# Performance work log

Measured on AMD Instinct MI355X. Metric: run time of the kernel, lower is better.

The kernel has to match this reference:

```python
import jax, jax.numpy as jnp
import numpy as np

B, L, S, T_IP = 2, 4096, 77, 16
C, C_CROSS, H = 1280, 768, 20
DH = C // H
REGION_WEIGHT = 0.3  # scalar inside weight_func: bias = region_state * sigma * REGION_WEIGHT
IP_SCALE = 1.0


def setup_inputs() -> dict:
    key = jax.random.key(0)
    ks = jax.random.split(key, 11)
    def w(k, shape, s=0.02):
        return jax.random.normal(k, shape, dtype=jnp.float32) * s
    return {
        "hidden_states": jax.random.normal(ks[0], (B, L, C), dtype=jnp.float32),
        "encoder_hidden_states": jax.random.normal(ks[1], (B, S, C_CROSS), dtype=jnp.float32),
        "ip_hidden_states": jax.random.normal(ks[2], (B, T_IP, C_CROSS), dtype=jnp.float32),
        "region_state": jax.random.uniform(ks[3], (B, L, S), dtype=jnp.float32),
        "sigma": jnp.full((1,), 14.6, dtype=jnp.float32),
        "Wq": w(ks[4], (C, C)),
        "Wk": w(ks[5], (C_CROSS, C)),
        "Wv": w(ks[6], (C_CROSS, C)),
        "Wk_ip": w(ks[7], (C_CROSS, C)),
        "Wv_ip": w(ks[8], (C_CROSS, C)),
        "Wout": w(ks[9], (C, C)),
        "b_out": jnp.zeros((C,), dtype=jnp.float32),
    }


def _split_heads(x):
    # [B, T, C] -> [B, H, T, DH]
    b, t, _ = x.shape
    return x.reshape(b, t, H, DH).transpose(0, 2, 1, 3)


def reference(hidden_states, encoder_hidden_states, ip_hidden_states, region_state,
              sigma, Wq, Wk, Wv, Wk_ip, Wv_ip, Wout, b_out):
    residual = hidden_states
    scale = 1.0 / np.sqrt(DH).astype(np.float32)

    q = _split_heads(hidden_states @ Wq)            # [B,H,L,DH]
    k = _split_heads(encoder_hidden_states @ Wk)    # [B,H,S,DH]
    v = _split_heads(encoder_hidden_states @ Wv)    # [B,H,S,DH]

    # region-state-biased cross attention (manual softmax path)
    scores = jnp.einsum('bhld,bhsd->bhls', q, k) * scale  # [B,H,L,S]
    # weight_func(region_state, sigma, attn_weight) -> region_state * sigma * REGION_WEIGHT,
    # broadcast over heads (repeat_interleave B -> B*H in the original).
    bias = (region_state * sigma[0] * REGION_WEIGHT)[:, None, :, :]  # [B,1,L,S]
    attn = jax.nn.softmax(scores + bias, axis=-1)
    out = jnp.einsum('bhls,bhsd->bhld', attn, v)
    out = out.transpose(0, 2, 1, 3).reshape(B, L, C)

    # IP-adapter stream: standard SDPA against image-prompt tokens
    k_ip = _split_heads(ip_hidden_states @ Wk_ip)   # [B,H,T,DH]
    v_ip = _split_heads(ip_hidden_states @ Wv_ip)
    s_ip = jax.nn.softmax(jnp.einsum('bhld,bhtd->bhlt', q, k_ip) * scale, axis=-1)
    out_ip = jnp.einsum('bhlt,bhtd->bhld', s_ip, v_ip).transpose(0, 2, 1, 3).reshape(B, L, C)

    out = out + IP_SCALE * out_ip
    out = out @ Wout + b_out     # attn.to_out[0]; to_out[1] is dropout (identity at p=0)
    return out + residual
```

## Files before the change

### kernel.cpp

```cpp
#include <hip/hip_runtime.h>
#include <cstdint>
#include <cstddef>

#define B_   2
#define L_   4096
#define S_   77
#define TIP_ 16
#define C_   1280
#define CC_  768
#define H_   20

typedef unsigned short u16;
typedef unsigned int   u32;
typedef __attribute__((ext_vector_type(8))) short bf16x8;
typedef __attribute__((ext_vector_type(8))) unsigned short u16x8;
typedef __attribute__((ext_vector_type(4))) float f32x4;

__device__ __forceinline__ u16 f2bf(float x) {
  u32 u = __float_as_uint(x);
  u32 r = (u + 0x7fffu + ((u >> 16) & 1u)) >> 16;
  return (u16)r;
}

__device__ __forceinline__ void gload16(const u16* g, const u16* l) {
  __builtin_amdgcn_global_load_lds(
      (const __attribute__((address_space(1))) u32*)g,
      (__attribute__((address_space(3))) u32*)(uintptr_t)l, 16, 0, 0);
}

__device__ __forceinline__ void wg_barrier() {
  asm volatile("s_barrier" ::: "memory");
}
template<int N>
__device__ __forceinline__ void vm_wait() {
  asm volatile("s_waitcnt vmcnt(%0)" :: "i"(N) : "memory");
}

__global__ __launch_bounds__(256) void prep_all(
    const float* __restrict__ X, const float* __restrict__ enc, const float* __restrict__ ip,
    u16* __restrict__ Xbf, u16* __restrict__ encbf, u16* __restrict__ ipbf,
    const float* __restrict__ Wq,  const float* __restrict__ Wk,   const float* __restrict__ Wv,
    const float* __restrict__ Wkip,const float* __restrict__ Wvip, const float* __restrict__ Wout,
    u16* __restrict__ WqT, u16* __restrict__ WkT, u16* __restrict__ WvT,
    u16* __restrict__ WkipT, u16* __restrict__ WvipT, u16* __restrict__ WoutT) {
  __shared__ float tile[32][33];
  const int bid = blockIdx.x;
  if (bid < 2048) {
    const int nX = B_*L_*C_;
    const int nE = B_*S_*CC_;
    const int nI = B_*TIP_*CC_;
    const int total4 = (nX + nE + nI) >> 2;
    for (int i = bid*256 + threadIdx.x; i < total4; i += 2048*256) {
      int idx = i << 2;
      const float* src; u16* dst; int off;
      if (idx < nX)            { src = X;   dst = Xbf;   off = idx; }
      else if (idx < nX + nE)  { src = enc; dst = encbf; off = idx - nX; }
      else                     { src = ip;  dst = ipbf;  off = idx - nX - nE; }
      float4 v = *(const float4*)(src + off);
      ushort4 o;
      o.x = f2bf(v.x); o.y = f2bf(v.y); o.z = f2bf(v.z); o.w = f2bf(v.w);
      *(ushort4*)(dst + off) = o;
    }
    return;
  }
  int t = bid - 2048;
  const float* src; u16* dst; int K;
  if      (t < 1600) { src = Wq;   dst = WqT;   K = C_;  }
  else if (t < 2560) { src = Wk;   dst = WkT;   K = CC_; t -= 1600; }
  else if (t < 3520) { src = Wv;   dst = WvT;   K = CC_; t -= 2560; }
  else if (t < 4480) { src = Wkip; dst = WkipT; K = CC_; t -= 3520; }
  else if (t < 5440) { src = Wvip; dst = WvipT; K = CC_; t -= 4480; }
  else               { src = Wout; dst = WoutT; K = C_;  t -= 5440; }
  const int tileK = t / 40, tileN = t % 40;
  const int tx = threadIdx.x & 31, ty = threadIdx.x >> 5;
  const int k0 = tileK*32, n0 = tileN*32;
  #pragma unroll
  for (int r = 0; r < 32; r += 8)
    tile[ty + r][tx] = src[(size_t)(k0 + ty + r)*C_ + n0 + tx];
  __syncthreads();
  #pragma unroll
  for (int r = 0; r < 32; r += 8) {
    const int n = n0 + ty + r, k = k0 + tx;
    dst[(size_t)n*K + k] = f2bf(tile[tx][ty + r]);
  }
}

template<int BM, int MODE, typename OutT>
__device__ __forceinline__ void gemm_core(
    const u16* __restrict__ A, int lda, int M,
    const u16* __restrict__ BT, int K,
    OutT* __restrict__ Cm,
    const float* __restrict__ bias, const float* __restrict__ resid,
    int mt, int nt) {
  constexpr int MR  = BM / 64;
  constexpr int AIT = BM / 64;
  constexpr int LP  = AIT + 3;
  __shared__ u16 As[2][BM*64];
  __shared__ u16 Bs[2][160*64];
  const int tid  = threadIdx.x;
  const int lane = tid & 63, wave = tid >> 6;
  const int wr = wave >> 1, wc = wave & 1;
  const int lhi = lane >> 4, llo = lane & 15;
  const int lsw = llo & 7;

  f32x4 acc[MR][5] = {};

  auto stage = [&](int kt) {
    u16* Asb = As[kt & 1];
    u16* Bsb = Bs[kt & 1];
    #pragma unroll
    for (int it = 0; it < AIT; ++it) {
      const int chunk = it*512 + wave*64 + lane;
      const int r = chunk >> 3, c8 = chunk & 7;
      const int g8 = c8 ^ (r & 7);
      int row_g = mt*BM + r; row_g = (row_g < M) ? row_g : (M - 1);
      gload16(A + (size_t)row_g*lda + kt*64 + g8*8,
              Asb + (size_t)(it*512 + wave*64)*8);
    }
    #pragma unroll
    for (int it = 0; it < 2; ++it) {
      const int chunk = it*512 + wave*64 + lane;
      const int r = chunk >> 3, c8 = chunk & 7;
      const int g8 = c8 ^ (r & 7);
      const int nrow = nt*160 + r;
      gload16(BT + (size_t)nrow*K + kt*64 + g8*8,
              Bsb + (size_t)(it*512 + wave*64)*8);
    }
    { const int chunk = 1024 + (wave & 3)*64 + lane;
      const int r = chunk >> 3, c8 = chunk & 7;
      const int g8 = c8 ^ (r & 7);
      const int nrow = nt*160 + r;
      gload16(BT + (size_t)nrow*K + kt*64 + g8*8,
              Bsb + (size_t)(1024 + (wave & 3)*64)*8);
    }
  };

  auto compute = [&](int kt) {
    const u16* Asb = As[kt & 1];
    const u16* Bsb = Bs[kt & 1];
    #pragma unroll
    for (int ks = 0; ks < 2; ++ks) {
      bf16x8 av[MR], bv[5];
      #pragma unroll
      for (int mm = 0; mm < MR; ++mm) {
        const int row = wr*(BM/4) + mm*16 + llo;
        av[mm] = *(const bf16x8*)(Asb + row*64 + (((ks*4 + lhi) ^ lsw) << 3));
      }
      #pragma unroll
      for (int nn = 0; nn < 5; ++nn) {
        const int row = wc*80 + nn*16 + llo;
        bv[nn] = *(const bf16x8*)(Bsb + row*64 + (((ks*4 + lhi) ^ lsw) << 3));
      }
      #pragma unroll
      for (int mm = 0; mm < MR; ++mm)
        #pragma unroll
        for (int nn = 0; nn < 5; ++nn)
          acc[mm][nn] = __builtin_amdgcn_mfma_f32_16x16x32_bf16(av[mm], bv[nn], acc[mm][nn], 0, 0, 0);
    }
  };

  const int nkt = K >> 6;
  stage(0);
  stage(1);
  vm_wait<LP>();
  wg_barrier();
  __builtin_amdgcn_sched_barrier(0);

  for (int kt = 0; kt < nkt; ++kt) {
    compute(kt);
    if (kt + 2 < nkt) {
      wg_barrier();
      stage(kt + 2);
      vm_wait<LP>();
      wg_barrier();
      __builtin_amdgcn_sched_barrier(0);
    } else if (kt + 1 < nkt) {
      vm_wait<0>();
      wg_barrier();
      __builtin_amdgcn_sched_barrier(0);
    }
  }

  #pragma unroll
  for (int mm = 0; mm < MR; ++mm) {
    #pragma unroll
    for (int nn = 0; nn < 5; ++nn) {
      const int row0 = mt*BM + wr*(BM/4) + mm*16 + lhi*4;
      const int col  = nt*160 + wc*80 + nn*16 + llo;
      #pragma unroll
      for (int r = 0; r < 4; ++r) {
        const int row = row0 + r;
        if (row < M) {
          float v = acc[mm][nn][r];
          if constexpr (MODE == 1) {
            v += bias[col] + resid[(size_t)row*C_ + col];
            Cm[(size_t)row*C_ + col] = v;
          } else {
            Cm[(size_t)row*C_ + col] = f2bf(v);
          }
        }
      }
    }
  }
}

template<int MODE, typename OutT>
__global__ __launch_bounds__(512, 2) void gemm_bf16(
    const u16* __restrict__ A, int lda, int M, const u16* __restrict__ BT, int K,
    OutT* __restrict__ Cm, const float* __restrict__ bias, const float* __restrict__ resid) {
  const int nwg = gridDim.x;
  const int bid = blockIdx.x;
  const int swz = (nwg & 7) ? bid : ((bid & 7) * (nwg >> 3) + (bid >> 3));
  gemm_core<256, MODE, OutT>(A, lda, M, BT, K, Cm, bias, resid, swz >> 3, swz & 7);
}

__global__ __launch_bounds__(512, 4) void gemm_small(
    const u16* __restrict__ encbf, const u16* __restrict__ ipbf,
    const u16* __restrict__ WkT, const u16* __restrict__ WvT,
    const u16* __restrict__ WkipT, const u16* __restrict__ WvipT,
    u16* __restrict__ Kbf, u16* __restrict__ Vbf,
    u16* __restrict__ Kipbf, u16* __restrict__ Vipbf) {
  const int zr = blockIdx.x >> 3, nt = blockIdx.x & 7;
  const u16* A; const u16* BT; u16* Cm; int M, mt;
  switch (zr) {
    case 0: A = encbf; BT = WkT;   Cm = Kbf;   M = B_*S_;   mt = 0; break;
    case 1: A = encbf; BT = WkT;   Cm = Kbf;   M = B_*S_;   mt = 1; break;
    case 2: A = encbf; BT = WvT;   Cm = Vbf;   M = B_*S_;   mt = 0; break;
    case 3: A = encbf; BT = WvT;   Cm = Vbf;   M = B_*S_;   mt = 1; break;
    case 4: A = ipbf;  BT = WkipT; Cm = Kipbf; M = B_*TIP_; mt = 0; break;
    default:A = ipbf;  BT = WvipT; Cm = Vipbf; M = B_*TIP_; mt = 0; break;
  }
  gemm_core<128, 2, u16>(A, CC_, M, BT, CC_, Cm, nullptr, nullptr, mt, nt);
}

#define KSP   96
#define KLD   72
#define PLD   100
__global__ __launch_bounds__(256) void attn_mfma(
    const u16* __restrict__ Qbf,
    const u16* __restrict__ Kbf,  const u16* __restrict__ Vbf,
    const u16* __restrict__ Kipbf, const u16* __restrict__ Vipbf,
    const float* __restrict__ region, const float* __restrict__ sigma,
    u16* __restrict__ attnbf) {
  __shared__ u16 Vt[64*PLD];
  __shared__ u16 R2[128*PLD];
  u16* Kl = R2;
  u16* Pl = R2;
  const int b = blockIdx.z, h = blockIdx.y;
  const int tid = threadIdx.x, lane = tid & 63, wave = tid >> 6;
  const int llo = lane & 15, lhi = lane >> 4;

  for (int i = tid; i < KSP*8; i += 256) {
    const int r = i >> 3, c8 = i & 7;
    u16x8 val = {0,0,0,0,0,0,0,0};
    if (r < S_)
      val = *(const u16x8*)(Kbf + ((size_t)(b*S_ + r))*C_ + h*64 + c8*8);
    else if (r >= 80)
      val = *(const u16x8*)(Kipbf + ((size_t)(b*TIP_ + r - 80))*C_ + h*64 + c8*8);
    *(u16x8*)(Kl + r*KLD + c8*8) = val;
  }
  for (int c = tid; c < KSP*8; c += 256) {
    const int s = c >> 3, d0 = (c & 7) * 8;
    u16x8 v = {0,0,0,0,0,0,0,0};
    if (s < S_)
      v = *(const u16x8*)(Vbf + ((size_t)(b*S_ + s))*C_ + h*64 + d0);
    else if (s >= 80)
      v = *(const u16x8*)(Vipbf + ((size_t)(b*TIP_ + s - 80))*C_ + h*64 + d0);
    #pragma unroll
    for (int j = 0; j < 8; ++j)
      Vt[(d0 + j)*PLD + s] = v[j];
  }
  __syncthreads();

  const int row0 = blockIdx.x*128 + wave*32;

  bf16x8 av[2][2];
  #pragma unroll
  for (int mm = 0; mm < 2; ++mm)
    #pragma unroll
    for (int ks = 0; ks < 2; ++ks)
      av[mm][ks] = *(const bf16x8*)(Qbf + ((size_t)(b*L_ + row0 + mm*16 + llo))*C_ + h*64 + ks*32 + lhi*8);

  f32x4 acc[2][6] = {};
  #pragma unroll
  for (int ks = 0; ks < 2; ++ks) {
    bf16x8 bv[6];
    #pragma unroll
    for (int nn = 0; nn < 6; ++nn)
      bv[nn] = *(const bf16x8*)(Kl + (nn*16 + llo)*KLD + ks*32 + lhi*8);
    #pragma unroll
    for (int mm = 0; mm < 2; ++mm)
      #pragma unroll
      for (int nn = 0; nn < 6; ++nn)
        acc[mm][nn] = __builtin_amdgcn_mfma_f32_16x16x32_bf16(av[mm][ks], bv[nn], acc[mm][nn], 0, 0, 0);
  }
  __syncthreads();

  const float sigscale = sigma[0] * 0.3f;
  const float scale = 0.125f;
  u16* Pw = Pl + wave*32*PLD;

  #pragma unroll
  for (int mm = 0; mm < 2; ++mm) {
    const int rowbase = b*L_ + row0 + mm*16 + lhi*4;
    float sc[5][4];
    float mx[4] = {-1e30f, -1e30f, -1e30f, -1e30f};
    #pragma unroll
    for (int nn = 0; nn < 5; ++nn) {
      const int col = nn*16 + llo;
      #pragma unroll
      for (int r = 0; r < 4; ++r) {
        float v = -1e30f;
        if (col < S_) {
          const float bias = region[((size_t)(rowbase + r))*S_ + col] * sigscale;
          v = fmaf(acc[mm][nn][r], scale, bias);
        }
        sc[nn][r] = v;
        mx[r] = fmaxf(mx[r], v);
      }
    }
    #pragma unroll
    for (int st = 1; st < 16; st <<= 1)
      #pragma unroll
      for (int r = 0; r < 4; ++r)
        mx[r] = fmaxf(mx[r], __shfl_xor(mx[r], st));
    float sum[4] = {0.f, 0.f, 0.f, 0.f};
    #pragma unroll
    for (int nn = 0; nn < 5; ++nn)
      #pragma unroll
      for (int r = 0; r < 4; ++r) {
        const float e = __expf(sc[nn][r] - mx[r]);
        sc[nn][r] = e; sum[r] += e;
      }
    #pragma unroll
    for (int st = 1; st < 16; st <<= 1)
      #pragma unroll
      for (int r = 0; r < 4; ++r)
        sum[r] += __shfl_xor(sum[r], st);
    float inv[4];
    #pragma unroll
    for (int r = 0; r < 4; ++r) inv[r] = 1.f / sum[r];

    float ipe[4], mi[4], sumi[4];
    #pragma unroll
    for (int r = 0; r < 4; ++r) { ipe[r] = acc[mm][5][r] * scale; mi[r] = ipe[r]; }
    #pragma unroll
    for (int st = 1; st < 16; st <<= 1)
      #pragma unroll
      for (int r = 0; r < 4; ++r)
        mi[r] = fmaxf(mi[r], __shfl_xor(mi[r], st));
    #pragma unroll
    for (int r = 0; r < 4; ++r) { ipe[r] = __expf(ipe[r] - mi[r]); sumi[r] = ipe[r]; }
    #pragma unroll
    for (int st = 1; st < 16; st <<= 1)
      #pragma unroll
      for (int r = 0; r < 4; ++r)
        sumi[r] += __shfl_xor(sumi[r], st);

    #pragma unroll
    for (int nn = 0; nn < 5; ++nn)
      #pragma unroll
      for (int r = 0; r < 4; ++r)
        Pw[(mm*16 + lhi*4 + r)*PLD + nn*16 + llo] = f2bf(sc[nn][r] * inv[r]);
    #pragma unroll
    for (int r = 0; r < 4; ++r)
      Pw[(mm*16 + lhi*4 + r)*PLD + 80 + llo] = f2bf(ipe[r] / sumi[r]);
  }

  f32x4 oacc[2][4] = {};
  #pragma unroll
  for (int ks = 0; ks < 3; ++ks) {
    bf16x8 pa[2], vv[4];
    #pragma unroll
    for (int mm = 0; mm < 2; ++mm)
      pa[mm] = *(const bf16x8*)(Pw + (mm*16 + llo)*PLD + ks*32 + lhi*8);
    #pragma unroll
    for (int nn = 0; nn < 4; ++nn)
      vv[nn] = *(const bf16x8*)(Vt + (nn*16 + llo)*PLD + ks*32 + lhi*8);
    #pragma unroll
    for (int mm = 0; mm < 2; ++mm)
      #pragma unroll
      for (int nn = 0; nn < 4; ++nn)
        oacc[mm][nn] = __builtin_amdgcn_mfma_f32_16x16x32_bf16(pa[mm], vv[nn], oacc[mm][nn], 0, 0, 0);
  }

  #pragma unroll
  for (int mm = 0; mm < 2; ++mm)
    #pragma unroll
    for (int nn = 0; nn < 4; ++nn)
      #pragma unroll
      for (int r = 0; r < 4; ++r) {
        const int grow = row0 + mm*16 + lhi*4 + r;
        attnbf[((size_t)(b*L_ + grow))*C_ + h*64 + nn*16 + llo] = f2bf(oacc[mm][nn][r]);
      }
}

extern "C" void kernel_launch(void* const* d_in, const int* in_sizes, int n_in,
                              void* d_out, int out_size, void* d_ws, size_t ws_size,
                              hipStream_t stream) {
  const float* hidden = (const float*)d_in[0];
  const float* enc    = (const float*)d_in[1];
  const float* ip     = (const float*)d_in[2];
  const float* region = (const float*)d_in[3];
  const float* sigma  = (const float*)d_in[4];
  const float* Wq     = (const float*)d_in[5];
  const float* Wk     = (const float*)d_in[6];
  const float* Wv     = (const float*)d_in[7];
  const float* Wkip   = (const float*)d_in[8];
  const float* Wvip   = (const float*)d_in[9];
  const float* Wout   = (const float*)d_in[10];
  const float* bout   = (const float*)d_in[11];

  char* base = (char*)d_ws;
  size_t off = 0;
  auto carve = [&](size_t bytes) -> void* {
    void* r = base + off;
    off += (bytes + 255) & ~(size_t)255;
    return r;
  };
  u16* Xbf    = (u16*)carve((size_t)B_*L_*C_*2);
  u16* encbf  = (u16*)carve((size_t)B_*S_*CC_*2);
  u16* ipbf   = (u16*)carve((size_t)B_*TIP_*CC_*2);
  u16* WqT    = (u16*)carve((size_t)C_*C_*2);
  u16* WkT    = (u16*)carve((size_t)C_*CC_*2);
  u16* WvT    = (u16*)carve((size_t)C_*CC_*2);
  u16* WkipT  = (u16*)carve((size_t)C_*CC_*2);
  u16* WvipT  = (u16*)carve((size_t)C_*CC_*2);
  u16* WoutT  = (u16*)carve((size_t)C_*C_*2);
  u16* Qbf    = (u16*)carve((size_t)B_*L_*C_*2);
  u16* Kbf    = (u16*)carve((size_t)B_*S_*C_*2);
  u16* Vbf    = (u16*)carve((size_t)B_*S_*C_*2);
  u16* Kipbf  = (u16*)carve((size_t)B_*TIP_*C_*2);
  u16* Vipbf  = (u16*)carve((size_t)B_*TIP_*C_*2);
  u16* attnbf = (u16*)carve((size_t)B_*L_*C_*2);
  (void)ws_size; (void)in_sizes; (void)n_in; (void)out_size;

  prep_all<<<dim3(2048 + 7040), 256, 0, stream>>>(
      hidden, enc, ip, Xbf, encbf, ipbf,
      Wq, Wk, Wv, Wkip, Wvip, Wout,
      WqT, WkT, WvT, WkipT, WvipT, WoutT);
  gemm_bf16<2, u16><<<dim3(256), 512, 0, stream>>>(Xbf, C_, B_*L_, WqT, C_, Qbf, nullptr, nullptr);
  gemm_small<<<dim3(48), 512, 0, stream>>>(encbf, ipbf, WkT, WvT, WkipT, WvipT,
                                           Kbf, Vbf, Kipbf, Vipbf);
  attn_mfma<<<dim3(L_/128, H_, B_), 256, 0, stream>>>(Qbf, Kbf, Vbf, Kipbf, Vipbf,
                                                      region, sigma, attnbf);
  gemm_bf16<1, float><<<dim3(256), 512, 0, stream>>>(attnbf, C_, B_*L_, WoutT, C_,
                                                     (float*)d_out, bout, hidden);
}
```

Measured before the change: 141.1 us.

## Fuse hidden-state bf16 conversion into Q GEMM A-load and shrink GEMM tiles

The Q projection GEMM now reads fp32 hidden states directly, converting to bf16 in registers before writing to LDS. This removes the separate conversion pass and the Xbf round trip through memory. The GEMM tile also shrinks from BM=256 to BM=128, which doubles the grid to 512 workgroups and raises the launch-bounds occupancy hint to 4. MFMA loops are wrapped in s_setprio. The register-staged fp32 load doubles A-side global traffic and loses the direct-to-LDS path, and the smaller tiles reduce reuse.

```diff
diff --git a/kernel.cpp b/kernel.cpp
--- a/kernel.cpp
+++ b/kernel.cpp
@@ -37,25 +37,23 @@
 }
 
 __global__ __launch_bounds__(256) void prep_all(
-    const float* __restrict__ X, const float* __restrict__ enc, const float* __restrict__ ip,
-    u16* __restrict__ Xbf, u16* __restrict__ encbf, u16* __restrict__ ipbf,
+    const float* __restrict__ enc, const float* __restrict__ ip,
+    u16* __restrict__ encbf, u16* __restrict__ ipbf,
     const float* __restrict__ Wq,  const float* __restrict__ Wk,   const float* __restrict__ Wv,
     const float* __restrict__ Wkip,const float* __restrict__ Wvip, const float* __restrict__ Wout,
     u16* __restrict__ WqT, u16* __restrict__ WkT, u16* __restrict__ WvT,
     u16* __restrict__ WkipT, u16* __restrict__ WvipT, u16* __restrict__ WoutT) {
   __shared__ float tile[32][33];
   const int bid = blockIdx.x;
-  if (bid < 2048) {
-    const int nX = B_*L_*C_;
+  if (bid < 64) {
     const int nE = B_*S_*CC_;
     const int nI = B_*TIP_*CC_;
-    const int total4 = (nX + nE + nI) >> 2;
-    for (int i = bid*256 + threadIdx.x; i < total4; i += 2048*256) {
+    const int total4 = (nE + nI) >> 2;
+    for (int i = bid*256 + threadIdx.x; i < total4; i += 64*256) {
       int idx = i << 2;
       const float* src; u16* dst; int off;
-      if (idx < nX)            { src = X;   dst = Xbf;   off = idx; }
-      else if (idx < nX + nE)  { src = enc; dst = encbf; off = idx - nX; }
-      else                     { src = ip;  dst = ipbf;  off = idx - nX - nE; }
+      if (idx < nE) { src = enc; dst = encbf; off = idx; }
+      else          { src = ip;  dst = ipbf;  off = idx - nE; }
       float4 v = *(const float4*)(src + off);
       ushort4 o;
       o.x = f2bf(v.x); o.y = f2bf(v.y); o.z = f2bf(v.z); o.w = f2bf(v.w);
@@ -63,7 +61,7 @@
     }
     return;
   }
-  int t = bid - 2048;
+  int t = bid - 64;
   const float* src; u16* dst; int K;
   if      (t < 1600) { src = Wq;   dst = WqT;   K = C_;  }
   else if (t < 2560) { src = Wk;   dst = WkT;   K = CC_; t -= 1600; }
@@ -85,16 +83,18 @@
   }
 }
 
-template<int BM, int MODE, typename OutT>
+template<int BM, int MODE, int AF32, typename OutT>
 __device__ __forceinline__ void gemm_core(
-    const u16* __restrict__ A, int lda, int M,
+    const void* __restrict__ Araw, int lda, int M,
     const u16* __restrict__ BT, int K,
     OutT* __restrict__ Cm,
     const float* __restrict__ bias, const float* __restrict__ resid,
     int mt, int nt) {
+  constexpr int AIT = BM / 64;
   constexpr int MR  = BM / 64;
-  constexpr int AIT = BM / 64;
   constexpr int LP  = AIT + 3;
+  const u16*   A  = (const u16*)Araw;
+  const float* Af = (const float*)Araw;
   __shared__ u16 As[2][BM*64];
   __shared__ u16 Bs[2][160*64];
   const int tid  = threadIdx.x;
@@ -105,9 +105,28 @@
 
   f32x4 acc[MR][5] = {};
 
-  auto stage = [&](int kt) {
+  auto bstage = [&](int kt) {
+    u16* Bsb = Bs[kt & 1];
+    #pragma unroll
+    for (int it = 0; it < 2; ++it) {
+      const int chunk = it*512 + wave*64 + lane;
+      const int r = chunk >> 3, c8 = chunk & 7;
+      const int g8 = c8 ^ (r & 7);
+      const int nrow = nt*160 + r;
+      gload16(BT + (size_t)nrow*K + kt*64 + g8*8,
+              Bsb + (size_t)(it*512 + wave*64)*8);
+    }
+    { const int chunk = 1024 + (wave & 3)*64 + lane;
+      const int r = chunk >> 3, c8 = chunk & 7;
+      const int g8 = c8 ^ (r & 7);
+      const int nrow = nt*160 + r;
+      gload16(BT + (size_t)nrow*K + kt*64 + g8*8,
+              Bsb + (size_t)(1024 + (wave & 3)*64)*8);
+    }
+  };
+
+  auto astage_dma = [&](int kt) {
     u16* Asb = As[kt & 1];
-    u16* Bsb = Bs[kt & 1];
     #pragma unroll
     for (int it = 0; it < AIT; ++it) {
       const int chunk = it*512 + wave*64 + lane;
@@ -117,21 +136,30 @@
       gload16(A + (size_t)row_g*lda + kt*64 + g8*8,
               Asb + (size_t)(it*512 + wave*64)*8);
     }
-    #pragma unroll
-    for (int it = 0; it < 2; ++it) {
+  };
+
+  auto aload_f32 = [&](int kt, float4 ar[AIT][2]) {
+    #pragma unroll
+    for (int it = 0; it < AIT; ++it) {
       const int chunk = it*512 + wave*64 + lane;
       const int r = chunk >> 3, c8 = chunk & 7;
       const int g8 = c8 ^ (r & 7);
-      const int nrow = nt*160 + r;
-      gload16(BT + (size_t)nrow*K + kt*64 + g8*8,
-              Bsb + (size_t)(it*512 + wave*64)*8);
-    }
-    { const int chunk = 1024 + (wave & 3)*64 + lane;
-      const int r = chunk >> 3, c8 = chunk & 7;
-      const int g8 = c8 ^ (r & 7);
-      const int nrow = nt*160 + r;
-      gload16(BT + (size_t)nrow*K + kt*64 + g8*8,
-              Bsb + (size_t)(1024 + (wave & 3)*64)*8);
+      int row_g = mt*BM + r; row_g = (row_g < M) ? row_g : (M - 1);
+      const float* src = Af + (size_t)row_g*lda + kt*64 + g8*8;
+      ar[it][0] = *(const float4*)src;
+      ar[it][1] = *(const float4*)(src + 4);
+    }
+  };
+  auto awrite_f32 = [&](int kt, float4 ar[AIT][2]) {
+    u16* Asb = As[kt & 1];
+    #pragma unroll
+    for (int it = 0; it < AIT; ++it) {
+      u16x8 o;
+      o[0] = f2bf(ar[it][0].x); o[1] = f2bf(ar[it][0].y);
+      o[2] = f2bf(ar[it][0].z); o[3] = f2bf(ar[it][0].w);
+      o[4] = f2bf(ar[it][1].x); o[5] = f2bf(ar[it][1].y);
+      o[6] = f2bf(ar[it][1].z); o[7] = f2bf(ar[it][1].w);
+      *(u16x8*)(Asb + (size_t)(it*512 + wave*64 + lane)*8) = o;
     }
   };
 
@@ -151,33 +179,65 @@
         const int row = wc*80 + nn*16 + llo;
         bv[nn] = *(const bf16x8*)(Bsb + row*64 + (((ks*4 + lhi) ^ lsw) << 3));
       }
+      __builtin_amdgcn_s_setprio(1);
       #pragma unroll
       for (int mm = 0; mm < MR; ++mm)
         #pragma unroll
         for (int nn = 0; nn < 5; ++nn)
           acc[mm][nn] = __builtin_amdgcn_mfma_f32_16x16x32_bf16(av[mm], bv[nn], acc[mm][nn], 0, 0, 0);
+      __builtin_amdgcn_s_setprio(0);
     }
   };
 
   const int nkt = K >> 6;
-  stage(0);
-  stage(1);
-  vm_wait<LP>();
-  wg_barrier();
-  __builtin_amdgcn_sched_barrier(0);
-
-  for (int kt = 0; kt < nkt; ++kt) {
-    compute(kt);
-    if (kt + 2 < nkt) {
-      wg_barrier();
-      stage(kt + 2);
-      vm_wait<LP>();
-      wg_barrier();
-      __builtin_amdgcn_sched_barrier(0);
-    } else if (kt + 1 < nkt) {
-      vm_wait<0>();
-      wg_barrier();
-      __builtin_amdgcn_sched_barrier(0);
+
+  if constexpr (AF32) {
+    float4 ar[AIT][2];
+    aload_f32(0, ar); bstage(0);
+    awrite_f32(0, ar);
+    aload_f32(1, ar); bstage(1);
+    awrite_f32(1, ar);
+    vm_wait<3>();
+    wg_barrier();
+    __builtin_amdgcn_sched_barrier(0);
+
+    for (int kt = 0; kt < nkt; ++kt) {
+      float4 ar2[AIT][2];
+      if (kt + 2 < nkt) aload_f32(kt + 2, ar2);
+      compute(kt);
+      if (kt + 2 < nkt) {
+        wg_barrier();
+        awrite_f32(kt + 2, ar2);
+        bstage(kt + 2);
+        vm_wait<3>();
+        wg_barrier();
+        __builtin_amdgcn_sched_barrier(0);
+      } else if (kt + 1 < nkt) {
+        vm_wait<0>();
+        wg_barrier();
+        __builtin_amdgcn_sched_barrier(0);
+      }
+    }
+  } else {
+    astage_dma(0); bstage(0);
+    astage_dma(1); bstage(1);
+    vm_wait<LP>();
+    wg_barrier();
+    __builtin_amdgcn_sched_barrier(0);
+
+    for (int kt = 0; kt < nkt; ++kt) {
+      compute(kt);
+      if (kt + 2 < nkt) {
+        wg_barrier();
+        astage_dma(kt + 2); bstage(kt + 2);
+        vm_wait<LP>();
+        wg_barrier();
+        __builtin_amdgcn_sched_barrier(0);
+      } else if (kt + 1 < nkt) {
+        vm_wait<0>();
+        wg_barrier();
+        __builtin_amdgcn_sched_barrier(0);
+      }
     }
   }
 
@@ -204,14 +264,14 @@
   }
 }
 
-template<int MODE, typename OutT>
-__global__ __launch_bounds__(512, 2) void gemm_bf16(
-    const u16* __restrict__ A, int lda, int M, const u16* __restrict__ BT, int K,
+template<int MODE, int AF32, typename OutT>
+__global__ __launch_bounds__(512, 4) void gemm_bf16(
+    const void* __restrict__ A, int lda, int M, const u16* __restrict__ BT, int K,
     OutT* __restrict__ Cm, const float* __restrict__ bias, const float* __restrict__ resid) {
   const int nwg = gridDim.x;
   const int bid = blockIdx.x;
   const int swz = (nwg & 7) ? bid : ((bid & 7) * (nwg >> 3) + (bid >> 3));
-  gemm_core<256, MODE, OutT>(A, lda, M, BT, K, Cm, bias, resid, swz >> 3, swz & 7);
+  gemm_core<128, MODE, AF32, OutT>(A, lda, M, BT, K, Cm, bias, resid, swz >> 3, swz & 7);
 }
 
 __global__ __launch_bounds__(512, 4) void gemm_small(
@@ -230,7 +290,7 @@
     case 4: A = ipbf;  BT = WkipT; Cm = Kipbf; M = B_*TIP_; mt = 0; break;
     default:A = ipbf;  BT = WvipT; Cm = Vipbf; M = B_*TIP_; mt = 0; break;
   }
-  gemm_core<128, 2, u16>(A, CC_, M, BT, CC_, Cm, nullptr, nullptr, mt, nt);
+  gemm_core<128, 2, 0, u16>(A, CC_, M, BT, CC_, Cm, nullptr, nullptr, mt, nt);
 }
 
 #define KSP   96
@@ -418,7 +478,6 @@
     off += (bytes + 255) & ~(size_t)255;
     return r;
   };
-  u16* Xbf    = (u16*)carve((size_t)B_*L_*C_*2);
   u16* encbf  = (u16*)carve((size_t)B_*S_*CC_*2);
   u16* ipbf   = (u16*)carve((size_t)B_*TIP_*CC_*2);
   u16* WqT    = (u16*)carve((size_t)C_*C_*2);
@@ -435,15 +494,15 @@
   u16* attnbf = (u16*)carve((size_t)B_*L_*C_*2);
   (void)ws_size; (void)in_sizes; (void)n_in; (void)out_size;
 
-  prep_all<<<dim3(2048 + 7040), 256, 0, stream>>>(
-      hidden, enc, ip, Xbf, encbf, ipbf,
+  prep_all<<<dim3(64 + 7040), 256, 0, stream>>>(
+      enc, ip, encbf, ipbf,
       Wq, Wk, Wv, Wkip, Wvip, Wout,
       WqT, WkT, WvT, WkipT, WvipT, WoutT);
-  gemm_bf16<2, u16><<<dim3(256), 512, 0, stream>>>(Xbf, C_, B_*L_, WqT, C_, Qbf, nullptr, nullptr);
+  gemm_bf16<2, 1, u16><<<dim3(512), 512, 0, stream>>>(hidden, C_, B_*L_, WqT, C_, Qbf, nullptr, nullptr);
   gemm_small<<<dim3(48), 512, 0, stream>>>(encbf, ipbf, WkT, WvT, WkipT, WvipT,
                                            Kbf, Vbf, Kipbf, Vipbf);
   attn_mfma<<<dim3(L_/128, H_, B_), 256, 0, stream>>>(Qbf, Kbf, Vbf, Kipbf, Vipbf,
                                                       region, sigma, attnbf);
-  gemm_bf16<1, float><<<dim3(256), 512, 0, stream>>>(attnbf, C_, B_*L_, WoutT, C_,
-                                                     (float*)d_out, bout, hidden);
-}
+  gemm_bf16<1, 0, float><<<dim3(512), 512, 0, stream>>>(attnbf, C_, B_*L_, WoutT, C_,
+                                                        (float*)d_out, bout, hidden);
+}
```

Measured after the change: 131.9 us. 1.07x faster.
